# Kernel optimization log

Hardware: AMD Instinct MI355X
Metric: run time of the kernel (lower is better)

The kernel has to match this reference:

```python
import jax, jax.numpy as jnp
import numpy as np

N = 100000      # nodes
E = 1600000     # edges (avg degree 16)
D_IN, D_H1, D_H2, D_OUT = 512, 256, 256, 64


def setup_inputs() -> dict:
    key = jax.random.key(0)
    ks = jax.random.split(key, 8)
    x = jax.random.normal(ks[0], (N, D_IN), dtype=jnp.float32)
    row = jax.random.randint(ks[1], (E,), 0, N, dtype=jnp.int32)
    col = jax.random.randint(ks[2], (E,), 0, N, dtype=jnp.int32)
    vals = jax.random.uniform(ks[3], (E,), dtype=jnp.float32)
    # xavier-normal-ish scaling for weights
    W1 = jax.random.normal(ks[4], (D_IN, D_H1), dtype=jnp.float32) * np.sqrt(2.0 / (D_IN + D_H1))
    W2 = jax.random.normal(ks[5], (D_H1, D_H2), dtype=jnp.float32) * np.sqrt(2.0 / (D_H1 + D_H2))
    W3 = jax.random.normal(ks[6], (D_H2, D_OUT), dtype=jnp.float32) * np.sqrt(2.0 / (D_H2 + D_OUT))
    b1 = jnp.zeros((D_H1,), dtype=jnp.float32)
    b2 = jnp.zeros((D_H2,), dtype=jnp.float32)
    b3 = jnp.zeros((D_OUT,), dtype=jnp.float32)
    return {"x": x, "row": row, "col": col, "vals": vals,
            "W1": W1, "b1": b1, "W2": W2, "b2": b2, "W3": W3, "b3": b3}


def reference(x, row, col, vals, W1, b1, W2, b2, W3, b3):
    n = x.shape[0]

    def spmm(h):
        # out[i] = sum_{e: row[e]==i} vals[e] * h[col[e]]  (COO spmm)
        return jax.ops.segment_sum(vals[:, None] * h[col], row, num_segments=n)

    # layer 1: linear -> spmm -> relu  (dropout p=0 -> identity)
    h = jax.nn.relu(spmm(x @ W1 + b1))
    # layer 2
    h = jax.nn.relu(spmm(h @ W2 + b2))
    # output layer: no activation, no dropout
    return spmm(h @ W3 + b3)
```

## Files before the change

kernel.cpp:

```cpp
#include <hip/hip_runtime.h>

typedef _Float16 f16;
typedef _Float16 f16x4 __attribute__((ext_vector_type(4)));
typedef _Float16 f16x8 __attribute__((ext_vector_type(8)));
typedef float f32x4 __attribute__((ext_vector_type(4)));

#define DEVI __device__ __forceinline__

static constexpr int CAP = 64;

DEVI f16x8 cvt8(float4 a, float4 b) {
  f16x8 r;
  r[0] = (f16)a.x; r[1] = (f16)a.y; r[2] = (f16)a.z; r[3] = (f16)a.w;
  r[4] = (f16)b.x; r[5] = (f16)b.y; r[6] = (f16)b.z; r[7] = (f16)b.w;
  return r;
}

__global__ __launch_bounds__(256)
void prep_w(const float* __restrict__ W1, const float* __restrict__ W2,
            const float* __restrict__ W3, f16* __restrict__ WT1,
            f16* __restrict__ WT2, f16* __restrict__ WT3) {
  int t = blockIdx.x * 256 + threadIdx.x;
  const float* W; f16* O; int N; int u;
  if (t < 16384) {
    W = W1; O = WT1; N = 256; u = t;
  } else if (t < 16384 + 8192) {
    W = W2; O = WT2; N = 256; u = t - 16384;
  } else if (t < 16384 + 8192 + 2048) {
    W = W3; O = WT3; N = 64;  u = t - 24576;
  } else return;
  const int per = (N >> 4) * 64;
  const int kc = u / per;
  const int rem = u - kc * per;
  const int l = rem & 63;
  const int n = ((rem >> 6) << 4) + (l & 15);
  const int kb = kc * 32 + ((l >> 4) << 3);
  f16x8 o;
#pragma unroll
  for (int j = 0; j < 8; ++j) o[j] = (f16)W[(size_t)(kb + j) * N + n];
  *(f16x8*)(O + (size_t)u * 8) = o;
}

__global__ __launch_bounds__(256)
void build_slots(const int* __restrict__ row, const int* __restrict__ col,
                 const float* __restrict__ vals, int* __restrict__ cnt,
                 int2* __restrict__ slots, int E) {
  int e = blockIdx.x * 256 + threadIdx.x;
  if (e >= E) return;
  int r = row[e];
  int p = atomicAdd(&cnt[r], 1);
  if (p < CAP) slots[(size_t)r * CAP + p] = make_int2(col[e], __float_as_int(vals[e]));
}

__global__ __launch_bounds__(256)
void gemm_l1_direct(const float* __restrict__ A, const f16* __restrict__ WT,
                    const float* __restrict__ bias, f16* __restrict__ C, int M) {
  constexpr int K = 512, N = 256, NF16 = N / 16;
  const int tid = threadIdx.x;
  const int wave = tid >> 6, lane = tid & 63;
  const int wm = wave >> 1, wn = wave & 1;
  const int quad = lane >> 4, l16 = lane & 15;
  const int r0 = blockIdx.x * 64 + wm * 32;

  const float* arow[2];
#pragma unroll
  for (int mt = 0; mt < 2; ++mt)
    arow[mt] = A + (size_t)min(r0 + mt * 16 + l16, M - 1) * K + quad * 8;

  f32x4 acc[2][8];
#pragma unroll
  for (int mt = 0; mt < 2; ++mt)
#pragma unroll
    for (int nt = 0; nt < 8; ++nt) {
      f32x4 z = {0.f, 0.f, 0.f, 0.f};
      acc[mt][nt] = z;
    }

#pragma unroll 2
  for (int kb = 0; kb < 16; ++kb) {
    f16x8 af[2], bf[8];
#pragma unroll
    for (int mt = 0; mt < 2; ++mt) {
      const float4* gp = (const float4*)(arow[mt] + kb * 32);
      float4 v0 = gp[0], v1 = gp[1];
      af[mt] = cvt8(v0, v1);
    }
#pragma unroll
    for (int nt = 0; nt < 8; ++nt) {
      int n16 = wn * 8 + nt;
      bf[nt] = *(const f16x8*)(WT + ((size_t)(kb * NF16 + n16) * 64 + lane) * 8);
    }
#pragma unroll
    for (int mt = 0; mt < 2; ++mt)
#pragma unroll
      for (int nt = 0; nt < 8; ++nt)
        acc[mt][nt] = __builtin_amdgcn_mfma_f32_16x16x32_f16(af[mt], bf[nt], acc[mt][nt], 0, 0, 0);
  }

  float bv[8];
#pragma unroll
  for (int nt = 0; nt < 8; ++nt) bv[nt] = bias[wn * 128 + nt * 16 + l16];
#pragma unroll
  for (int mt = 0; mt < 2; ++mt) {
#pragma unroll
    for (int nt = 0; nt < 8; ++nt) {
      int colg = wn * 128 + nt * 16 + l16;
#pragma unroll
      for (int r = 0; r < 4; ++r) {
        int grow = r0 + mt * 16 + quad * 4 + r;
        if (grow < M)
          C[(size_t)grow * N + colg] = (f16)(acc[mt][nt][r] + bv[nt]);
      }
    }
  }
}

template <int NTILES>
__global__ __launch_bounds__(256)
void gemm_direct(const f16* __restrict__ A, const f16* __restrict__ WT,
                 const float* __restrict__ bias, f16* __restrict__ C, int M) {
  constexpr int K = 256, N = NTILES * 64, NF16 = N / 16;
  const int tid = threadIdx.x;
  const int wave = tid >> 6, lane = tid & 63;
  const int quad = lane >> 4, l16 = lane & 15;
  const int gw = blockIdx.x * 4 + wave;
  const int mtile = (NTILES == 1) ? gw : (gw / NTILES);
  const int ntile = (NTILES == 1) ? 0 : (gw % NTILES);
  const int r0 = mtile * 64;
  if (r0 >= M) return;

  size_t arow[4];
#pragma unroll
  for (int mt = 0; mt < 4; ++mt)
    arow[mt] = (size_t)min(r0 + mt * 16 + l16, M - 1) * K;

  f32x4 acc[4][4];
#pragma unroll
  for (int mt = 0; mt < 4; ++mt)
#pragma unroll
    for (int nt = 0; nt < 4; ++nt) {
      f32x4 z = {0.f, 0.f, 0.f, 0.f};
      acc[mt][nt] = z;
    }

#pragma unroll
  for (int kb = 0; kb < 8; ++kb) {
    f16x8 af[4], bf[4];
#pragma unroll
    for (int mt = 0; mt < 4; ++mt)
      af[mt] = *(const f16x8*)(A + arow[mt] + kb * 32 + quad * 8);
#pragma unroll
    for (int nt = 0; nt < 4; ++nt) {
      int n16 = ntile * 4 + nt;
      bf[nt] = *(const f16x8*)(WT + ((size_t)(kb * NF16 + n16) * 64 + lane) * 8);
    }
#pragma unroll
    for (int mt = 0; mt < 4; ++mt)
#pragma unroll
      for (int nt = 0; nt < 4; ++nt)
        acc[mt][nt] = __builtin_amdgcn_mfma_f32_16x16x32_f16(af[mt], bf[nt], acc[mt][nt], 0, 0, 0);
  }

  float bv[4];
#pragma unroll
  for (int nt = 0; nt < 4; ++nt) bv[nt] = bias[ntile * 64 + nt * 16 + l16];
#pragma unroll
  for (int mt = 0; mt < 4; ++mt) {
#pragma unroll
    for (int nt = 0; nt < 4; ++nt) {
      int colg = ntile * 64 + nt * 16 + l16;
#pragma unroll
      for (int r = 0; r < 4; ++r) {
        int grow = r0 + mt * 16 + quad * 4 + r;
        if (grow < M)
          C[(size_t)grow * N + colg] = (f16)(acc[mt][nt][r] + bv[nt]);
      }
    }
  }
}

__global__ __launch_bounds__(256)
void spmm_relu256(const f16* __restrict__ T, const int2* __restrict__ slots,
                  const int* __restrict__ cnt, f16* __restrict__ H, int nrows) {
  const int wave = threadIdx.x >> 6, lane = threadIdx.x & 63;
  const int i = blockIdx.x * 4 + wave;
  if (i >= nrows) return;
  const int c = min(cnt[i], CAP);
  const int2* sl = slots + (size_t)i * CAP;
  float a0 = 0.f, a1 = 0.f, a2 = 0.f, a3 = 0.f;
  int j = 0;
  for (; j + 4 <= c; j += 4) {
    int2 e0 = sl[j], e1 = sl[j + 1], e2 = sl[j + 2], e3 = sl[j + 3];
    f16x4 u0 = ((const f16x4*)(T + (size_t)e0.x * 256))[lane];
    f16x4 u1 = ((const f16x4*)(T + (size_t)e1.x * 256))[lane];
    f16x4 u2 = ((const f16x4*)(T + (size_t)e2.x * 256))[lane];
    f16x4 u3 = ((const f16x4*)(T + (size_t)e3.x * 256))[lane];
    float v0 = __int_as_float(e0.y), v1 = __int_as_float(e1.y);
    float v2 = __int_as_float(e2.y), v3 = __int_as_float(e3.y);
    a0 += v0 * (float)u0.x + v1 * (float)u1.x + v2 * (float)u2.x + v3 * (float)u3.x;
    a1 += v0 * (float)u0.y + v1 * (float)u1.y + v2 * (float)u2.y + v3 * (float)u3.y;
    a2 += v0 * (float)u0.z + v1 * (float)u1.z + v2 * (float)u2.z + v3 * (float)u3.z;
    a3 += v0 * (float)u0.w + v1 * (float)u1.w + v2 * (float)u2.w + v3 * (float)u3.w;
  }
  for (; j < c; ++j) {
    int2 e = sl[j];
    f16x4 u = ((const f16x4*)(T + (size_t)e.x * 256))[lane];
    float v = __int_as_float(e.y);
    a0 += v * (float)u.x; a1 += v * (float)u.y;
    a2 += v * (float)u.z; a3 += v * (float)u.w;
  }
  f16x4 o;
  o.x = (f16)fmaxf(a0, 0.f); o.y = (f16)fmaxf(a1, 0.f);
  o.z = (f16)fmaxf(a2, 0.f); o.w = (f16)fmaxf(a3, 0.f);
  ((f16x4*)(H + (size_t)i * 256))[lane] = o;
}

__global__ __launch_bounds__(256)
void spmm_out64(const f16* __restrict__ T, const int2* __restrict__ slots,
                const int* __restrict__ cnt, float* __restrict__ out, int nrows) {
  const int wave = threadIdx.x >> 6, lane = threadIdx.x & 63;
  const int i = blockIdx.x * 4 + wave;
  if (i >= nrows) return;
  const int c = min(cnt[i], CAP);
  const int2* sl = slots + (size_t)i * CAP;
  float a = 0.f;
  int j = 0;
  for (; j + 4 <= c; j += 4) {
    int2 e0 = sl[j], e1 = sl[j + 1], e2 = sl[j + 2], e3 = sl[j + 3];
    float u0 = (float)T[(size_t)e0.x * 64 + lane];
    float u1 = (float)T[(size_t)e1.x * 64 + lane];
    float u2 = (float)T[(size_t)e2.x * 64 + lane];
    float u3 = (float)T[(size_t)e3.x * 64 + lane];
    a += __int_as_float(e0.y) * u0 + __int_as_float(e1.y) * u1
       + __int_as_float(e2.y) * u2 + __int_as_float(e3.y) * u3;
  }
  for (; j < c; ++j) {
    int2 e = sl[j];
    a += __int_as_float(e.y) * (float)T[(size_t)e.x * 64 + lane];
  }
  out[(size_t)i * 64 + lane] = a;
}

extern "C" void kernel_launch(void* const* d_in, const int* in_sizes, int n_in,
                              void* d_out, int out_size, void* d_ws, size_t ws_size,
                              hipStream_t stream) {
  const float* x    = (const float*)d_in[0];
  const int*   row  = (const int*)d_in[1];
  const int*   col  = (const int*)d_in[2];
  const float* vals = (const float*)d_in[3];
  const float* W1   = (const float*)d_in[4];
  const float* b1   = (const float*)d_in[5];
  const float* W2   = (const float*)d_in[6];
  const float* b2   = (const float*)d_in[7];
  const float* W3   = (const float*)d_in[8];
  const float* b3   = (const float*)d_in[9];
  float* out = (float*)d_out;

  const int N = in_sizes[0] / 512;
  const int E = in_sizes[1];

  char* ws = (char*)d_ws;
  const size_t MiB = 1ull << 20;
  int*  cnt   = (int*)ws;
  int2* slots = (int2*)(ws + 1 * MiB);
  f16*  WT1   = (f16*)(ws + 52 * MiB);
  f16*  WT2   = WT1 + 256 * 512;
  f16*  WT3   = WT2 + 256 * 256;
  f16*  T     = (f16*)(ws + 53 * MiB);
  f16*  H     = (f16*)(ws + 104 * MiB);

  hipMemsetAsync(cnt, 0, (size_t)N * sizeof(int), stream);
  prep_w<<<(16384 + 8192 + 2048 + 255) / 256, 256, 0, stream>>>(W1, W2, W3, WT1, WT2, WT3);
  build_slots<<<(E + 255) / 256, 256, 0, stream>>>(row, col, vals, cnt, slots, E);

  const int mt64 = (N + 63) / 64;
  dim3 gs((N + 3) / 4);

  gemm_l1_direct<<<mt64, 256, 0, stream>>>(x, WT1, b1, T, N);
  spmm_relu256<<<gs, 256, 0, stream>>>(T, slots, cnt, H, N);
  gemm_direct<4><<<mt64, 256, 0, stream>>>(H, WT2, b2, T, N);
  spmm_relu256<<<gs, 256, 0, stream>>>(T, slots, cnt, H, N);
  gemm_direct<1><<<(mt64 + 3) / 4, 256, 0, stream>>>(H, WT3, b3, T, N);
  spmm_out64<<<gs, 256, 0, stream>>>(T, slots, cnt, out, N);
}
```

Baseline: 836.1 us.

## Double-buffer GEMM operand loads and deepen SpMM gather unrolling

The GEMM kernels now prefetch the next k-block's A and B fragments into register double buffers while the MFMAs run on the current block, and both GEMMs get a min-blocks-per-CU hint of 2 in their launch bounds. The SpMM kernels gather eight neighbor rows per iteration instead of four, so more independent loads are in flight. The goal is to hide global memory latency in both stages. The extra live registers could cause spills or lower occupancy.

```diff
diff --git a/kernel.cpp b/kernel.cpp
--- a/kernel.cpp
+++ b/kernel.cpp
@@ -52,20 +52,19 @@
   if (p < CAP) slots[(size_t)r * CAP + p] = make_int2(col[e], __float_as_int(vals[e]));
 }
 
-__global__ __launch_bounds__(256)
+__global__ __launch_bounds__(256, 2)
 void gemm_l1_direct(const float* __restrict__ A, const f16* __restrict__ WT,
                     const float* __restrict__ bias, f16* __restrict__ C, int M) {
-  constexpr int K = 512, N = 256, NF16 = N / 16;
+  constexpr int K = 512, N = 256;
   const int tid = threadIdx.x;
   const int wave = tid >> 6, lane = tid & 63;
   const int wm = wave >> 1, wn = wave & 1;
   const int quad = lane >> 4, l16 = lane & 15;
   const int r0 = blockIdx.x * 64 + wm * 32;
 
-  const float* arow[2];
-#pragma unroll
-  for (int mt = 0; mt < 2; ++mt)
-    arow[mt] = A + (size_t)min(r0 + mt * 16 + l16, M - 1) * K + quad * 8;
+  const float4* ap0 = (const float4*)(A + (size_t)min(r0 + l16, M - 1) * K + quad * 8);
+  const float4* ap1 = (const float4*)(A + (size_t)min(r0 + 16 + l16, M - 1) * K + quad * 8);
+  const f16x8* bp = (const f16x8*)WT + (size_t)(wn * 8) * 64 + lane;
 
   f32x4 acc[2][8];
 #pragma unroll
@@ -76,26 +75,35 @@
       acc[mt][nt] = z;
     }
 
-#pragma unroll 2
+  float4 ab[2][2][2];
+  f16x8 bb[2][8];
+
+#define L1_LOAD(P, KB)                                   \
+  ab[P][0][0] = ap0[(KB) * 8];                           \
+  ab[P][0][1] = ap0[(KB) * 8 + 1];                       \
+  ab[P][1][0] = ap1[(KB) * 8];                           \
+  ab[P][1][1] = ap1[(KB) * 8 + 1];                       \
+  {                                                      \
+    _Pragma("unroll")                                    \
+    for (int nt = 0; nt < 8; ++nt)                       \
+      bb[P][nt] = bp[((KB) * 16 + nt) * 64];             \
+  }
+
+  L1_LOAD(0, 0)
+#pragma unroll
   for (int kb = 0; kb < 16; ++kb) {
-    f16x8 af[2], bf[8];
-#pragma unroll
-    for (int mt = 0; mt < 2; ++mt) {
-      const float4* gp = (const float4*)(arow[mt] + kb * 32);
-      float4 v0 = gp[0], v1 = gp[1];
-      af[mt] = cvt8(v0, v1);
-    }
-#pragma unroll
-    for (int nt = 0; nt < 8; ++nt) {
-      int n16 = wn * 8 + nt;
-      bf[nt] = *(const f16x8*)(WT + ((size_t)(kb * NF16 + n16) * 64 + lane) * 8);
-    }
-#pragma unroll
-    for (int mt = 0; mt < 2; ++mt)
-#pragma unroll
-      for (int nt = 0; nt < 8; ++nt)
-        acc[mt][nt] = __builtin_amdgcn_mfma_f32_16x16x32_f16(af[mt], bf[nt], acc[mt][nt], 0, 0, 0);
-  }
+    const int cur = kb & 1, nxt = cur ^ 1;
+    if (kb + 1 < 16) { L1_LOAD(nxt, kb + 1) }
+    f16x8 af0 = cvt8(ab[cur][0][0], ab[cur][0][1]);
+    f16x8 af1 = cvt8(ab[cur][1][0], ab[cur][1][1]);
+#pragma unroll
+    for (int nt = 0; nt < 8; ++nt)
+      acc[0][nt] = __builtin_amdgcn_mfma_f32_16x16x32_f16(af0, bb[cur][nt], acc[0][nt], 0, 0, 0);
+#pragma unroll
+    for (int nt = 0; nt < 8; ++nt)
+      acc[1][nt] = __builtin_amdgcn_mfma_f32_16x16x32_f16(af1, bb[cur][nt], acc[1][nt], 0, 0, 0);
+  }
+#undef L1_LOAD
 
   float bv[8];
 #pragma unroll
@@ -116,7 +124,7 @@
 }
 
 template <int NTILES>
-__global__ __launch_bounds__(256)
+__global__ __launch_bounds__(256, 2)
 void gemm_direct(const f16* __restrict__ A, const f16* __restrict__ WT,
                  const float* __restrict__ bias, f16* __restrict__ C, int M) {
   constexpr int K = 256, N = NTILES * 64, NF16 = N / 16;
@@ -129,10 +137,11 @@
   const int r0 = mtile * 64;
   if (r0 >= M) return;
 
-  size_t arow[4];
-#pragma unroll
-  for (int mt = 0; mt < 4; ++mt)
-    arow[mt] = (size_t)min(r0 + mt * 16 + l16, M - 1) * K;
+  const f16x8* ap0 = (const f16x8*)(A + (size_t)min(r0 + l16, M - 1) * K) + quad;
+  const f16x8* ap1 = (const f16x8*)(A + (size_t)min(r0 + 16 + l16, M - 1) * K) + quad;
+  const f16x8* ap2 = (const f16x8*)(A + (size_t)min(r0 + 32 + l16, M - 1) * K) + quad;
+  const f16x8* ap3 = (const f16x8*)(A + (size_t)min(r0 + 48 + l16, M - 1) * K) + quad;
+  const f16x8* bp = (const f16x8*)WT + (size_t)(ntile * 4) * 64 + lane;
 
   f32x4 acc[4][4];
 #pragma unroll
@@ -143,23 +152,31 @@
       acc[mt][nt] = z;
     }
 
+  f16x8 ab[2][4], bb[2][4];
+
+#define GD_LOAD(P, KB)                                   \
+  ab[P][0] = ap0[(KB) * 4];                              \
+  ab[P][1] = ap1[(KB) * 4];                              \
+  ab[P][2] = ap2[(KB) * 4];                              \
+  ab[P][3] = ap3[(KB) * 4];                              \
+  {                                                      \
+    _Pragma("unroll")                                    \
+    for (int nt = 0; nt < 4; ++nt)                       \
+      bb[P][nt] = bp[((KB) * NF16 + nt) * 64];           \
+  }
+
+  GD_LOAD(0, 0)
 #pragma unroll
   for (int kb = 0; kb < 8; ++kb) {
-    f16x8 af[4], bf[4];
+    const int cur = kb & 1, nxt = cur ^ 1;
+    if (kb + 1 < 8) { GD_LOAD(nxt, kb + 1) }
 #pragma unroll
     for (int mt = 0; mt < 4; ++mt)
-      af[mt] = *(const f16x8*)(A + arow[mt] + kb * 32 + quad * 8);
-#pragma unroll
-    for (int nt = 0; nt < 4; ++nt) {
-      int n16 = ntile * 4 + nt;
-      bf[nt] = *(const f16x8*)(WT + ((size_t)(kb * NF16 + n16) * 64 + lane) * 8);
-    }
-#pragma unroll
-    for (int mt = 0; mt < 4; ++mt)
 #pragma unroll
       for (int nt = 0; nt < 4; ++nt)
-        acc[mt][nt] = __builtin_amdgcn_mfma_f32_16x16x32_f16(af[mt], bf[nt], acc[mt][nt], 0, 0, 0);
-  }
+        acc[mt][nt] = __builtin_amdgcn_mfma_f32_16x16x32_f16(ab[cur][mt], bb[cur][nt], acc[mt][nt], 0, 0, 0);
+  }
+#undef GD_LOAD
 
   float bv[4];
 #pragma unroll
@@ -189,20 +206,32 @@
   const int2* sl = slots + (size_t)i * CAP;
   float a0 = 0.f, a1 = 0.f, a2 = 0.f, a3 = 0.f;
   int j = 0;
-  for (; j + 4 <= c; j += 4) {
-    int2 e0 = sl[j], e1 = sl[j + 1], e2 = sl[j + 2], e3 = sl[j + 3];
+  for (; j + 8 <= c; j += 8) {
+    int2 e[8];
+#pragma unroll
+    for (int q = 0; q < 8; ++q) e[q] = sl[j + q];
+    f16x4 u[8];
+#pragma unroll
+    for (int q = 0; q < 8; ++q)
+      u[q] = ((const f16x4*)(T + (size_t)e[q].x * 256))[lane];
+#pragma unroll
+    for (int q = 0; q < 8; ++q) {
+      float v = __int_as_float(e[q].y);
+      a0 += v * (float)u[q].x; a1 += v * (float)u[q].y;
+      a2 += v * (float)u[q].z; a3 += v * (float)u[q].w;
+    }
+  }
+  for (; j + 2 <= c; j += 2) {
+    int2 e0 = sl[j], e1 = sl[j + 1];
     f16x4 u0 = ((const f16x4*)(T + (size_t)e0.x * 256))[lane];
     f16x4 u1 = ((const f16x4*)(T + (size_t)e1.x * 256))[lane];
-    f16x4 u2 = ((const f16x4*)(T + (size_t)e2.x * 256))[lane];
-    f16x4 u3 = ((const f16x4*)(T + (size_t)e3.x * 256))[lane];
     float v0 = __int_as_float(e0.y), v1 = __int_as_float(e1.y);
-    float v2 = __int_as_float(e2.y), v3 = __int_as_float(e3.y);
-    a0 += v0 * (float)u0.x + v1 * (float)u1.x + v2 * (float)u2.x + v3 * (float)u3.x;
-    a1 += v0 * (float)u0.y + v1 * (float)u1.y + v2 * (float)u2.y + v3 * (float)u3.y;
-    a2 += v0 * (float)u0.z + v1 * (float)u1.z + v2 * (float)u2.z + v3 * (float)u3.z;
-    a3 += v0 * (float)u0.w + v1 * (float)u1.w + v2 * (float)u2.w + v3 * (float)u3.w;
-  }
-  for (; j < c; ++j) {
+    a0 += v0 * (float)u0.x + v1 * (float)u1.x;
+    a1 += v0 * (float)u0.y + v1 * (float)u1.y;
+    a2 += v0 * (float)u0.z + v1 * (float)u1.z;
+    a3 += v0 * (float)u0.w + v1 * (float)u1.w;
+  }
+  if (j < c) {
     int2 e = sl[j];
     f16x4 u = ((const f16x4*)(T + (size_t)e.x * 256))[lane];
     float v = __int_as_float(e.y);
@@ -225,14 +254,15 @@
   const int2* sl = slots + (size_t)i * CAP;
   float a = 0.f;
   int j = 0;
-  for (; j + 4 <= c; j += 4) {
-    int2 e0 = sl[j], e1 = sl[j + 1], e2 = sl[j + 2], e3 = sl[j + 3];
-    float u0 = (float)T[(size_t)e0.x * 64 + lane];
-    float u1 = (float)T[(size_t)e1.x * 64 + lane];
-    float u2 = (float)T[(size_t)e2.x * 64 + lane];
-    float u3 = (float)T[(size_t)e3.x * 64 + lane];
-    a += __int_as_float(e0.y) * u0 + __int_as_float(e1.y) * u1
-       + __int_as_float(e2.y) * u2 + __int_as_float(e3.y) * u3;
+  for (; j + 8 <= c; j += 8) {
+    int2 e[8];
+#pragma unroll
+    for (int q = 0; q < 8; ++q) e[q] = sl[j + q];
+    float u[8];
+#pragma unroll
+    for (int q = 0; q < 8; ++q) u[q] = (float)T[(size_t)e[q].x * 64 + lane];
+#pragma unroll
+    for (int q = 0; q < 8; ++q) a += __int_as_float(e[q].y) * u[q];
   }
   for (; j < c; ++j) {
     int2 e = sl[j];
```

After: 845.5 us. No clear change (+1.1%).
